# Kernel tuning notes

Measured on AMD Instinct MI355X. Metric: run time of the kernel, lower is better.

Reference implementation:

```python
import jax, jax.numpy as jnp
import numpy as np

B, N, D = 4, 4096, 256


def setup_inputs() -> dict:
    key = jax.random.key(0)
    ks = jax.random.split(key, 7)
    s = 1.0 / np.sqrt(D)
    return {
        "x": jax.random.normal(ks[0], (B, N, D), dtype=jnp.float32),
        "Wq": jax.random.normal(ks[1], (D, D), dtype=jnp.float32) * s,
        "bq": jax.random.normal(ks[2], (D,), dtype=jnp.float32) * 0.01,
        "Wk": jax.random.normal(ks[3], (D, D), dtype=jnp.float32) * s,
        "bk": jax.random.normal(ks[4], (D,), dtype=jnp.float32) * 0.01,
        "Wv": jax.random.normal(ks[5], (D, D), dtype=jnp.float32) * s,
        "bv": jax.random.normal(ks[6], (D,), dtype=jnp.float32) * 0.01,
    }


def reference(x, Wq, bq, Wk, bk, Wv, bv):
    # nn.Linear: y = x @ W.T + b
    q = jnp.einsum("bnd,ed->bne", x, Wq) + bq
    k = jnp.einsum("bnd,ed->bne", x, Wk) + bk
    v = jnp.einsum("bnd,ed->bne", x, Wv) + bv
    n = x.shape[1]
    # causal mask: -inf above diagonal, 0 on/below (as in create_masking)
    mask = jnp.where(
        jnp.tril(jnp.ones((n, n), dtype=bool)), 0.0, -jnp.inf
    ).astype(x.dtype)
    # NOTE: source applies NO 1/sqrt(d) scaling
    scores = jnp.einsum("bqd,bkd->bqk", q, k) + mask
    attn = jax.nn.softmax(scores, axis=-1)
    return jnp.einsum("bqk,bkd->bqd", attn, v)
```

## Files before the change

kernel.cpp:

```cpp
#include <hip/hip_runtime.h>
#include <hip/hip_bf16.h>


#define SEQ   4096
#define DIM   256
#define LOG2E 1.4426950408889634f

typedef _Float16 f16;
typedef __attribute__((ext_vector_type(8)))  f16    f16x8;
typedef __attribute__((ext_vector_type(16))) float  f32x16;

__global__ __launch_bounds__(256) void wsplit_h(
    const float* __restrict__ Wq, const float* __restrict__ Wk,
    const float* __restrict__ Wv, f16* __restrict__ whq,
    f16* __restrict__ whk, f16* __restrict__ whv)
{
    const float* W; f16* wh;
    if (blockIdx.y == 0)      { W = Wq; wh = whq; }
    else if (blockIdx.y == 1) { W = Wk; wh = whk; }
    else                      { W = Wv; wh = whv; }
    const int i = blockIdx.x * 256 + threadIdx.x;
    wh[i] = (f16)W[i];
}

__global__ __launch_bounds__(256) void proj3(
    const float* __restrict__ X,
    const f16* __restrict__ Whq, const float* __restrict__ bq,
    const f16* __restrict__ Whk, const float* __restrict__ bk,
    const f16* __restrict__ Whv, const float* __restrict__ bv,
    f16* __restrict__ outq, f16* __restrict__ outk, f16* __restrict__ outv)
{
    __shared__ f16 vtile[64][264];

    const f16* Wh; const float* bias; float scale;
    if (blockIdx.y == 0)      { Wh = Whq; bias = bq; scale = LOG2E; }
    else if (blockIdx.y == 1) { Wh = Whk; bias = bk; scale = 1.f; }
    else                      { Wh = Whv; bias = bv; scale = 1.f; }

    const int w = threadIdx.x >> 6, lane = threadIdx.x & 63;
    const int col = lane & 31, hi = lane >> 5;
    const int m0 = blockIdx.x * 64 + (w & 1) * 32;
    const int e0 = (w >> 1) * 128;

    f32x16 acc[4] = {};
    for (int s = 0; s < 16; ++s) {
        const float* xp = X + (size_t)(m0 + col) * DIM + s * 16 + 8 * hi;
        float xv[8];
        *(float4*)&xv[0] = *(const float4*)xp;
        *(float4*)&xv[4] = *(const float4*)(xp + 4);
        f16x8 xh;
        #pragma unroll
        for (int i = 0; i < 8; ++i) xh[i] = (f16)xv[i];
        #pragma unroll
        for (int c = 0; c < 4; ++c) {
            const size_t wo = (size_t)(e0 + c * 32 + col) * DIM + s * 16 + 8 * hi;
            const f16x8 wh = *(const f16x8*)(Wh + wo);
            acc[c] = __builtin_amdgcn_mfma_f32_32x32x16_f16(xh, wh, acc[c], 0, 0, 0);
        }
    }

    if (blockIdx.y < 2) {
        const int bb = m0 >> 12;
        const int m0loc = m0 & 4095;
        f16* fp = (blockIdx.y == 0 ? outq : outk)
                  + (size_t)bb * SEQ * DIM + (size_t)(m0loc >> 5) * 8192;
        #pragma unroll
        for (int c = 0; c < 4; ++c) {
            const int e = e0 + c * 32 + col;
            const float b = bias[e];
            const int eo = (e >> 4) * 512 + ((e >> 3) & 1) * 256 + (e & 7);
            #pragma unroll
            for (int r = 0; r < 16; ++r) {
                const int qr = (r & 3) + 8 * (r >> 2) + 4 * hi;
                fp[eo + qr * 8] = (f16)((acc[c][r] + b) * scale);
            }
        }
    } else {
        #pragma unroll
        for (int c = 0; c < 4; ++c) {
            const int e = e0 + c * 32 + col;
            const float b = bias[e];
            #pragma unroll
            for (int r = 0; r < 16; ++r) {
                const int qr = (r & 3) + 8 * (r >> 2) + 4 * hi;
                vtile[32 * (w & 1) + qr][e] = (f16)(acc[c][r] + b);
            }
        }
        __syncthreads();
        const int bb   = blockIdx.x >> 6;
        const int kb   = (blockIdx.x & 63) >> 1;
        const int half = blockIdx.x & 1;
        uint4* vout = (uint4*)outv + (size_t)bb * 131072;
        const int tid = threadIdx.x;
        const int slr = tid >> 6, l = tid & 63;
        const int row = 16 * slr + 8 * (l >> 5);
        #pragma unroll
        for (int i = 0; i < 8; ++i) {
            f16 tmp[8];
            #pragma unroll
            for (int j = 0; j < 8; ++j)
                tmp[j] = vtile[row + j][32 * i + (l & 31)];
            vout[(size_t)(8 * kb + i) * 512 + (4 * half + slr) * 64 + l] =
                *(const uint4*)tmp;
        }
    }
}

__global__ __launch_bounds__(256, 1) void attn_flash14(
    const uint4* __restrict__ qfrag, const uint4* __restrict__ kfrag,
    const uint4* __restrict__ vfrag, float* __restrict__ out, int nb)
{
    __shared__ uint4 Pex[2][512];
    __shared__ float mlbuf[2][2][4][32];

    int qt, b;
    if (nb == 4) {
        const int lin = blockIdx.x;
        const int x = lin & 7;
        b = x >> 1;
        const int k = lin >> 3;
        const int f = (k < 32) ? k : (95 - k);
        qt = 2 * f + (x & 1);
    } else { qt = blockIdx.x; b = 0; }

    const size_t pp = (size_t)SEQ * DIM;
    const uint4* qfb = qfrag + (size_t)b * 131072;
    const uint4* kfb = kfrag + (size_t)b * 131072;
    const uint4* vfb = vfrag + (size_t)b * 131072;
    float* outb = out + b * pp;

    const int wid = threadIdx.x >> 6, lane = threadIdx.x & 63;
    const int col = lane & 31, hi = lane >> 5;
    const int kq = wid;
    const int q0 = qt * 32;
    const int nt = (qt + 4) >> 2;

    f16x8 qhf[16];
    {
        const uint4* qp = qfb + (size_t)(q0 >> 5) * 1024 + lane;
        #pragma unroll
        for (int sl = 0; sl < 16; ++sl)
            qhf[sl] = __builtin_bit_cast(f16x8, qp[sl * 64]);
    }

    float m_run = -1e28f, l_run = 0.f;
    f32x16 oacc[2] = {};

    for (int t = 0; t < nt; ++t) {
        const int key0 = t << 7;
        const int pb = t & 1;
        const uint4* kp = kfb + (size_t)(4 * t + kq) * 1024 + lane;

        f32x16 s1 = {}, s2 = {};
        #pragma unroll
        for (int sl = 0; sl < 16; ++sl) {
            const f16x8 kf = __builtin_bit_cast(f16x8, kp[sl * 64]);
            if (sl & 1) s2 = __builtin_amdgcn_mfma_f32_32x32x16_f16(kf, qhf[sl], s2, 0, 0, 0);
            else        s1 = __builtin_amdgcn_mfma_f32_32x32x16_f16(kf, qhf[sl], s1, 0, 0, 0);
        }

        const uint4* vp = vfb + (size_t)(8 * t + 2 * kq) * 512 + lane;
        f16x8 vfA[2][4];
        #pragma unroll
        for (int cg = 0; cg < 2; ++cg)
            #pragma unroll
            for (int s = 0; s < 4; ++s)
                vfA[cg][s] = __builtin_bit_cast(f16x8, vp[cg * 512 + s * 64]);

        float sv[16];
        float pmax = -1e30f, tsum = 0.f;
        #pragma unroll
        for (int r = 0; r < 16; ++r) {
            const int kg = key0 + 32 * kq + (r & 3) + 8 * (r >> 2) + 4 * hi;
            const float x = (kg <= q0 + col) ? (s1[r] + s2[r]) : -1e30f;
            sv[r] = x;
            pmax = fmaxf(pmax, x);
        }
        pmax = fmaxf(pmax, __shfl_xor(pmax, 32));
        pmax = fmaxf(pmax, -1e28f);
        {
            float p[16];
            #pragma unroll
            for (int r = 0; r < 16; ++r) {
                p[r] = exp2f(sv[r] - pmax);
                tsum += p[r];
            }
            tsum += __shfl_xor(tsum, 32);
            uint32_t Wd[8], Od[8];
            #pragma unroll
            for (int jj = 0; jj < 8; ++jj)
                Wd[jj] = __builtin_bit_cast(uint32_t,
                    __builtin_amdgcn_cvt_pkrtz(p[2 * jj], p[2 * jj + 1]));
            #pragma unroll
            for (int jj = 0; jj < 8; ++jj)
                Od[jj] = (uint32_t)__shfl_xor((int)Wd[jj], 32);
            uint4 A0, A1;
            if (hi == 0) {
                A0.x = Wd[0]; A0.y = Wd[1]; A0.z = Od[0]; A0.w = Od[1];
                A1.x = Wd[4]; A1.y = Wd[5]; A1.z = Od[4]; A1.w = Od[5];
            } else {
                A0.x = Od[2]; A0.y = Od[3]; A0.z = Wd[2]; A0.w = Wd[3];
                A1.x = Od[6]; A1.y = Od[7]; A1.z = Wd[6]; A1.w = Wd[7];
            }
            Pex[pb][((2 * kq + 0) * 2 + hi) * 32 + col] = A0;
            Pex[pb][((2 * kq + 1) * 2 + hi) * 32 + col] = A1;
        }
        if (lane < 32) {
            mlbuf[pb][0][kq][col] = pmax;
            mlbuf[pb][1][kq][col] = tsum;
        }

        f16x8 vfB[2][4];
        #pragma unroll
        for (int cg = 0; cg < 2; ++cg)
            #pragma unroll
            for (int s = 0; s < 4; ++s)
                vfB[cg][s] = __builtin_bit_cast(f16x8, vp[cg * 512 + (s + 4) * 64]);

        __syncthreads();

        const float mw0 = mlbuf[pb][0][0][col], mw1 = mlbuf[pb][0][1][col];
        const float mw2 = mlbuf[pb][0][2][col], mw3 = mlbuf[pb][0][3][col];
        const float tw0 = mlbuf[pb][1][0][col], tw1 = mlbuf[pb][1][1][col];
        const float tw2 = mlbuf[pb][1][2][col], tw3 = mlbuf[pb][1][3][col];
        const float mt = fmaxf(fmaxf(mw0, mw1), fmaxf(mw2, mw3));
        float scale = 1.f;
        if (__any(mt > m_run + 11.5415603f)) {
            const float m_new = fmaxf(m_run, mt);
            scale = exp2f(m_run - m_new);
            m_run = m_new;
            #pragma unroll
            for (int r = 0; r < 16; ++r) {
                const int qr = (r & 3) + 8 * (r >> 2) + 4 * hi;
                const float scr = __shfl(scale, qr | (lane & 32));
                oacc[0][r] *= scr; oacc[1][r] *= scr;
            }
        }
        const float c0 = exp2f(mw0 - m_run), c1 = exp2f(mw1 - m_run);
        const float c2 = exp2f(mw2 - m_run), c3 = exp2f(mw3 - m_run);
        l_run = l_run * scale + tw0 * c0 + tw1 * c1 + tw2 * c2 + tw3 * c3;
        const f16 ch[4] = {(f16)c0, (f16)c1, (f16)c2, (f16)c3};

        #pragma unroll
        for (int s4 = 0; s4 < 4; ++s4) {
            f16x8 af = __builtin_bit_cast(f16x8, Pex[pb][(s4 * 2 + hi) * 32 + col]);
            af = af * ch[s4 >> 1];
            oacc[0] = __builtin_amdgcn_mfma_f32_32x32x16_f16(af, vfA[0][s4], oacc[0], 0, 0, 0);
            oacc[1] = __builtin_amdgcn_mfma_f32_32x32x16_f16(af, vfA[1][s4], oacc[1], 0, 0, 0);
        }
        #pragma unroll
        for (int s4 = 0; s4 < 4; ++s4) {
            f16x8 af = __builtin_bit_cast(f16x8, Pex[pb][((s4 + 4) * 2 + hi) * 32 + col]);
            af = af * ch[2 + (s4 >> 1)];
            oacc[0] = __builtin_amdgcn_mfma_f32_32x32x16_f16(af, vfB[0][s4], oacc[0], 0, 0, 0);
            oacc[1] = __builtin_amdgcn_mfma_f32_32x32x16_f16(af, vfB[1][s4], oacc[1], 0, 0, 0);
        }
    }

    const float linv = 1.f / l_run;
    #pragma unroll
    for (int r = 0; r < 16; ++r) {
        const int qr = (r & 3) + 8 * (r >> 2) + 4 * hi;
        const float lr = __shfl(linv, qr | (lane & 32));
        const int n = q0 + qr;
        outb[(size_t)n * DIM + 64 * kq + col]      = oacc[0][r] * lr;
        outb[(size_t)n * DIM + 64 * kq + 32 + col] = oacc[1][r] * lr;
    }
}

extern "C" void kernel_launch(void* const* d_in, const int* in_sizes, int n_in,
                              void* d_out, int out_size, void* d_ws, size_t ws_size,
                              hipStream_t stream) {
    const float* x  = (const float*)d_in[0];
    const float* Wq = (const float*)d_in[1];
    const float* bq = (const float*)d_in[2];
    const float* Wk = (const float*)d_in[3];
    const float* bk = (const float*)d_in[4];
    const float* Wv = (const float*)d_in[5];
    const float* bv = (const float*)d_in[6];
    float* out = (float*)d_out;

    const size_t PP = (size_t)SEQ * DIM;
    const size_t FULL = 4 * PP;
    const size_t WSZ = (size_t)DIM * DIM;

    if (ws_size >= FULL * 2 * 5) {
        f16* qfr = (f16*)d_ws;
        f16* kfr = qfr + FULL;
        f16* vfr = kfr + FULL;
        f16* whq = vfr + FULL;
        f16* whk = whq + WSZ;
        f16* whv = whk + WSZ;

        wsplit_h<<<dim3(256, 3), 256, 0, stream>>>(Wq, Wk, Wv, whq, whk, whv);
        proj3<<<dim3(256, 3), 256, 0, stream>>>(
            x, whq, bq, whk, bk, whv, bv, qfr, kfr, vfr);
        attn_flash14<<<dim3(512), 256, 0, stream>>>(
            (const uint4*)qfr, (const uint4*)kfr, (const uint4*)vfr, out, 4);
    } else {
        f16* qfr = (f16*)d_ws;
        f16* kfr = qfr + PP;
        f16* vfr = kfr + PP;
        f16* whq = vfr + PP;
        f16* whk = whq + WSZ;
        f16* whv = whk + WSZ;

        wsplit_h<<<dim3(256, 3), 256, 0, stream>>>(Wq, Wk, Wv, whq, whk, whv);
        for (int b = 0; b < 4; ++b) {
            const float* xb = x + b * PP;
            proj3<<<dim3(64, 3), 256, 0, stream>>>(
                xb, whq, bq, whk, bk, whv, bv, qfr, kfr, vfr);
            attn_flash14<<<dim3(128), 256, 0, stream>>>(
                (const uint4*)qfr, (const uint4*)kfr, (const uint4*)vfr, out + b * PP, 1);
        }
    }
}
```

Measured before the change: 126.6 us.

## Compute Q, K and V projections in one block per 32-row tile

The projection kernel is restructured so each block handles 32 rows and loops over all three weight matrices, rather than launching a separate grid dimension per projection over 64-row tiles. Each wave now covers 64 output columns instead of 128, and the V transpose layout is adapted to the 32-row tile. The aim is to reuse the X rows (through cache) across Q, K and V and to cut register pressure. The cost is serialising the three projections inside one block, which leaves only 512 blocks in total.

```diff
diff --git a/kernel.cpp b/kernel.cpp
--- a/kernel.cpp
+++ b/kernel.cpp
@@ -23,85 +23,88 @@
     wh[i] = (f16)W[i];
 }
 
-__global__ __launch_bounds__(256) void proj3(
+__global__ __launch_bounds__(256) void proj_all2(
     const float* __restrict__ X,
-    const f16* __restrict__ Whq, const float* __restrict__ bq,
-    const f16* __restrict__ Whk, const float* __restrict__ bk,
-    const f16* __restrict__ Whv, const float* __restrict__ bv,
+    const f16* __restrict__ whq, const float* __restrict__ bq,
+    const f16* __restrict__ whk, const float* __restrict__ bk,
+    const f16* __restrict__ whv, const float* __restrict__ bv,
     f16* __restrict__ outq, f16* __restrict__ outk, f16* __restrict__ outv)
 {
-    __shared__ f16 vtile[64][264];
-
-    const f16* Wh; const float* bias; float scale;
-    if (blockIdx.y == 0)      { Wh = Whq; bias = bq; scale = LOG2E; }
-    else if (blockIdx.y == 1) { Wh = Whk; bias = bk; scale = 1.f; }
-    else                      { Wh = Whv; bias = bv; scale = 1.f; }
+    __shared__ f16 vtile[32][264];
 
     const int w = threadIdx.x >> 6, lane = threadIdx.x & 63;
     const int col = lane & 31, hi = lane >> 5;
-    const int m0 = blockIdx.x * 64 + (w & 1) * 32;
-    const int e0 = (w >> 1) * 128;
-
-    f32x16 acc[4] = {};
-    for (int s = 0; s < 16; ++s) {
-        const float* xp = X + (size_t)(m0 + col) * DIM + s * 16 + 8 * hi;
-        float xv[8];
-        *(float4*)&xv[0] = *(const float4*)xp;
-        *(float4*)&xv[4] = *(const float4*)(xp + 4);
-        f16x8 xh;
-        #pragma unroll
-        for (int i = 0; i < 8; ++i) xh[i] = (f16)xv[i];
-        #pragma unroll
-        for (int c = 0; c < 4; ++c) {
-            const size_t wo = (size_t)(e0 + c * 32 + col) * DIM + s * 16 + 8 * hi;
-            const f16x8 wh = *(const f16x8*)(Wh + wo);
-            acc[c] = __builtin_amdgcn_mfma_f32_32x32x16_f16(xh, wh, acc[c], 0, 0, 0);
-        }
-    }
-
-    if (blockIdx.y < 2) {
-        const int bb = m0 >> 12;
-        const int m0loc = m0 & 4095;
-        f16* fp = (blockIdx.y == 0 ? outq : outk)
-                  + (size_t)bb * SEQ * DIM + (size_t)(m0loc >> 5) * 8192;
-        #pragma unroll
-        for (int c = 0; c < 4; ++c) {
-            const int e = e0 + c * 32 + col;
-            const float b = bias[e];
-            const int eo = (e >> 4) * 512 + ((e >> 3) & 1) * 256 + (e & 7);
-            #pragma unroll
-            for (int r = 0; r < 16; ++r) {
-                const int qr = (r & 3) + 8 * (r >> 2) + 4 * hi;
-                fp[eo + qr * 8] = (f16)((acc[c][r] + b) * scale);
-            }
-        }
-    } else {
-        #pragma unroll
-        for (int c = 0; c < 4; ++c) {
-            const int e = e0 + c * 32 + col;
-            const float b = bias[e];
-            #pragma unroll
-            for (int r = 0; r < 16; ++r) {
-                const int qr = (r & 3) + 8 * (r >> 2) + 4 * hi;
-                vtile[32 * (w & 1) + qr][e] = (f16)(acc[c][r] + b);
-            }
-        }
-        __syncthreads();
-        const int bb   = blockIdx.x >> 6;
-        const int kb   = (blockIdx.x & 63) >> 1;
-        const int half = blockIdx.x & 1;
-        uint4* vout = (uint4*)outv + (size_t)bb * 131072;
-        const int tid = threadIdx.x;
-        const int slr = tid >> 6, l = tid & 63;
-        const int row = 16 * slr + 8 * (l >> 5);
-        #pragma unroll
-        for (int i = 0; i < 8; ++i) {
-            f16 tmp[8];
-            #pragma unroll
-            for (int j = 0; j < 8; ++j)
-                tmp[j] = vtile[row + j][32 * i + (l & 31)];
-            vout[(size_t)(8 * kb + i) * 512 + (4 * half + slr) * 64 + l] =
-                *(const uint4*)tmp;
+    const int m0 = blockIdx.x * 32;
+    const int bb = blockIdx.x >> 7;
+    const int g  = blockIdx.x & 127;
+    const int e0 = w * 64;
+
+    #pragma unroll 1
+    for (int p = 0; p < 3; ++p) {
+        const f16* Wh = (p == 0) ? whq : (p == 1) ? whk : whv;
+        const float* bias = (p == 0) ? bq : (p == 1) ? bk : bv;
+
+        f32x16 acc[2] = {};
+        for (int s = 0; s < 16; ++s) {
+            const float* xp = X + (size_t)(m0 + col) * DIM + s * 16 + 8 * hi;
+            float xv[8];
+            *(float4*)&xv[0] = *(const float4*)xp;
+            *(float4*)&xv[4] = *(const float4*)(xp + 4);
+            f16x8 xh;
+            #pragma unroll
+            for (int i = 0; i < 8; ++i) xh[i] = (f16)xv[i];
+            #pragma unroll
+            for (int c = 0; c < 2; ++c) {
+                const size_t wo = (size_t)(e0 + c * 32 + col) * DIM + s * 16 + 8 * hi;
+                const f16x8 wh = *(const f16x8*)(Wh + wo);
+                acc[c] = __builtin_amdgcn_mfma_f32_32x32x16_f16(xh, wh, acc[c], 0, 0, 0);
+            }
+        }
+
+        if (p < 2) {
+            const float scale = (p == 0) ? LOG2E : 1.f;
+            f16* fp = (p == 0 ? outq : outk)
+                      + (size_t)bb * SEQ * DIM + (size_t)g * 8192;
+            #pragma unroll
+            for (int c = 0; c < 2; ++c) {
+                const int e = e0 + c * 32 + col;
+                const float b = bias[e];
+                const int eo = (e >> 4) * 512 + ((e >> 3) & 1) * 256 + (e & 7);
+                #pragma unroll
+                for (int r = 0; r < 16; ++r) {
+                    const int qr = (r & 3) + 8 * (r >> 2) + 4 * hi;
+                    fp[eo + qr * 8] = (f16)((acc[c][r] + b) * scale);
+                }
+            }
+        } else {
+            #pragma unroll
+            for (int c = 0; c < 2; ++c) {
+                const int e = e0 + c * 32 + col;
+                const float b = bias[e];
+                #pragma unroll
+                for (int r = 0; r < 16; ++r) {
+                    const int qr = (r & 3) + 8 * (r >> 2) + 4 * hi;
+                    vtile[qr][e] = (f16)(acc[c][r] + b);
+                }
+            }
+            __syncthreads();
+            const int kb = g >> 2;
+            const int qq = g & 3;
+            uint4* vout = (uint4*)outv + (size_t)bb * 131072;
+            #pragma unroll
+            for (int ii = 0; ii < 4; ++ii) {
+                const int e = threadIdx.x + 256 * ii;
+                const int db = e >> 7;
+                const int sl2 = (e >> 6) & 1;
+                const int l = e & 63;
+                const int kr = 16 * sl2 + 8 * (l >> 5);
+                f16 tmp[8];
+                #pragma unroll
+                for (int j = 0; j < 8; ++j)
+                    tmp[j] = vtile[kr + j][32 * db + (l & 31)];
+                vout[(size_t)(8 * kb + db) * 512 + (2 * qq + sl2) * 64 + l] =
+                    *(const uint4*)tmp;
+            }
         }
     }
 }
@@ -293,7 +296,7 @@
         f16* whv = whk + WSZ;
 
         wsplit_h<<<dim3(256, 3), 256, 0, stream>>>(Wq, Wk, Wv, whq, whk, whv);
-        proj3<<<dim3(256, 3), 256, 0, stream>>>(
+        proj_all2<<<dim3(512), 256, 0, stream>>>(
             x, whq, bq, whk, bk, whv, bv, qfr, kfr, vfr);
         attn_flash14<<<dim3(512), 256, 0, stream>>>(
             (const uint4*)qfr, (const uint4*)kfr, (const uint4*)vfr, out, 4);
@@ -308,7 +311,7 @@
         wsplit_h<<<dim3(256, 3), 256, 0, stream>>>(Wq, Wk, Wv, whq, whk, whv);
         for (int b = 0; b < 4; ++b) {
             const float* xb = x + b * PP;
-            proj3<<<dim3(64, 3), 256, 0, stream>>>(
+            proj_all2<<<dim3(128), 256, 0, stream>>>(
                 xb, whq, bq, whk, bk, whv, bv, qfr, kfr, vfr);
             attn_flash14<<<dim3(128), 256, 0, stream>>>(
                 (const uint4*)qfr, (const uint4*)kfr, (const uint4*)vfr, out + b * PP, 1);
```

Measured after the change: 133.5 us. 5.4% more time.
